# Kernel tuning notes

Hardware: AMD Instinct MI355X
Metric: run time of the kernel (lower is better)

Reference implementation:

```python
import jax, jax.numpy as jnp
import numpy as np

N, E, F, H, L = 100000, 800000, 128, 128, 64


def _glorot(key, shape):
    lim = float(np.sqrt(6.0 / (shape[0] + shape[1])))
    return jax.random.uniform(key, shape, jnp.float32, -lim, lim)


def setup_inputs() -> dict:
    key = jax.random.key(0)
    ks = jax.random.split(key, 10)
    x = jax.random.normal(ks[0], (N, F), jnp.float32)
    noise = jax.random.normal(ks[1], (N, F), jnp.float32)
    edge_index = jax.random.randint(ks[2], (2, E), 0, N, jnp.int32)
    return {
        "x": x,
        "noise": noise,
        "edge_index": edge_index,
        "bn_gamma": jnp.ones((F,), jnp.float32),
        "bn_beta": jnp.zeros((F,), jnp.float32),
        "W1": _glorot(ks[3], (F, H)),
        "b1": jnp.zeros((H,), jnp.float32),
        "W2": _glorot(ks[4], (H + 2 * F, H)),
        "b2": jnp.zeros((H,), jnp.float32),
        "Wm": _glorot(ks[5], (H + F, L)),
        "bm": jnp.zeros((L,), jnp.float32),
        "Ws": _glorot(ks[6], (H + F, L)),
        "bs": jnp.zeros((L,), jnp.float32),
    }


def _gcn_conv(x, W, b, src, dst, norm, n):
    # GCNConv: transform, then sym-normalized sparse aggregation, then bias
    h = x @ W                                 # [n, out]
    msg = h[src] * norm[:, None]              # gather + scale  [E', out]
    return jax.ops.segment_sum(msg, dst, num_segments=n) + b


def reference(x, noise, edge_index, bn_gamma, bn_beta, W1, b1, W2, b2, Wm, bm, Ws, bs):
    n = x.shape[0]
    loops = jnp.arange(n, dtype=edge_index.dtype)
    src = jnp.concatenate([edge_index[0], loops])  # add self-loops
    dst = jnp.concatenate([edge_index[1], loops])
    deg = jax.ops.segment_sum(jnp.ones_like(src, dtype=x.dtype), dst, num_segments=n)
    dinv = jnp.where(deg > 0, jax.lax.rsqrt(jnp.maximum(deg, 1e-12)), 0.0)
    norm = dinv[src] * dinv[dst]                   # D^-1/2 A D^-1/2 edge weights

    # bn1 (training-mode batch norm over nodes)
    mu = x.mean(axis=0)
    var = x.var(axis=0)
    xb = (x - mu) * jax.lax.rsqrt(var + 1e-5) * bn_gamma + bn_beta

    h1 = jax.nn.relu(_gcn_conv(xb, W1, b1, src, dst, norm, n))
    h1 = jnp.concatenate([xb, noise, h1], axis=1)  # [n, H + 2F]
    h2 = jax.nn.relu(_gcn_conv(h1, W2, b2, src, dst, norm, n))
    # dropout(p=0.4) in eval mode -> identity
    last = jnp.concatenate([xb, h2], axis=1)       # [n, F + H]
    z_mean = _gcn_conv(last, Wm, bm, src, dst, norm, n)
    z_logstd = _gcn_conv(last, Ws, bs, src, dst, norm, n)
    return (z_mean, z_logstd)
```

## Files before the change

### kernel.cpp

```cpp
#include <hip/hip_runtime.h>
#include <math.h>


typedef short bf16x8 __attribute__((ext_vector_type(8)));
typedef float f32x4 __attribute__((ext_vector_type(4)));

#define BN_G 1024

__device__ inline unsigned short f2bf(float f) {
    unsigned int u = __builtin_bit_cast(unsigned int, f);
    u += 0x7fff + ((u >> 16) & 1);
    return (unsigned short)(u >> 16);
}
__device__ inline float bfl(unsigned int u) { return __builtin_bit_cast(float, u << 16); }
__device__ inline float bfh(unsigned int u) { return __builtin_bit_cast(float, u & 0xffff0000u); }
__device__ inline unsigned int pack2(float lo, float hi) {
    return ((unsigned int)f2bf(hi) << 16) | f2bf(lo);
}
__device__ inline void acc8(float* a, uint4 v) {
    a[0] += bfl(v.x); a[1] += bfh(v.x);
    a[2] += bfl(v.y); a[3] += bfh(v.y);
    a[4] += bfl(v.z); a[5] += bfh(v.z);
    a[6] += bfl(v.w); a[7] += bfh(v.w);
}

__device__ __forceinline__ void gload_lds16(const void* g, void* l) {
    __builtin_amdgcn_global_load_lds(
        (const __attribute__((address_space(1))) unsigned int*)g,
        (__attribute__((address_space(3))) unsigned int*)l, 16, 0, 0);
}

__global__ void zero_i32(int* __restrict__ p, int n) {
    int i = blockIdx.x * blockDim.x + threadIdx.x;
    if (i < n) p[i] = 0;
}

__global__ void count_deg(const int* __restrict__ ei, int* __restrict__ cnt,
                          int* __restrict__ slot, int E) {
    int e = blockIdx.x * blockDim.x + threadIdx.x;
    if (e < E) slot[e] = atomicAdd(&cnt[ei[E + e]], 1);
}

__global__ void dinv_from_cnt(const int* __restrict__ cnt, float* __restrict__ dinv, int n) {
    int i = blockIdx.x * blockDim.x + threadIdx.x;
    if (i < n) dinv[i] = rsqrtf((float)cnt[i] + 1.0f);
}

#define SCAN_BLK 256
#define SCAN_ELEMS 1024

__global__ void scan_blocks(const int* __restrict__ cnt, int* __restrict__ out,
                            int* __restrict__ bsums, int n) {
    __shared__ int lds[SCAN_BLK];
    int base = blockIdx.x * SCAN_ELEMS;
    int t = threadIdx.x;
    int v[4];
    int s = 0;
#pragma unroll
    for (int j = 0; j < 4; j++) {
        int i = base + t * 4 + j;
        v[j] = s;
        s += (i < n) ? cnt[i] : 0;
    }
    lds[t] = s;
    __syncthreads();
    for (int off = 1; off < SCAN_BLK; off <<= 1) {
        int val = (t >= off) ? lds[t - off] : 0;
        __syncthreads();
        lds[t] += val;
        __syncthreads();
    }
    int excl = (t == 0) ? 0 : lds[t - 1];
#pragma unroll
    for (int j = 0; j < 4; j++) {
        int i = base + t * 4 + j;
        if (i < n) out[i] = excl + v[j];
    }
    if (t == SCAN_BLK - 1) bsums[blockIdx.x] = lds[t];
}

__global__ void scan_bsums(int* __restrict__ bsums, int nb) {
    if (threadIdx.x == 0 && blockIdx.x == 0) {
        int acc = 0;
        for (int i = 0; i < nb; i++) { int c = bsums[i]; bsums[i] = acc; acc += c; }
    }
}

__global__ void scan_add(int* __restrict__ row_ptr, const int* __restrict__ bsums, int n, int E) {
    int i = blockIdx.x * blockDim.x + threadIdx.x;
    if (i < n) row_ptr[i] += bsums[i / SCAN_ELEMS];
    if (i == 0) row_ptr[n] = E;
}

__global__ void fill_edges(const int* __restrict__ ei, const int* __restrict__ row_ptr,
                           const int* __restrict__ slot, int* __restrict__ edge_src, int E) {
    int e = blockIdx.x * blockDim.x + threadIdx.x;
    if (e >= E) return;
    int s = ei[e], d = ei[E + e];
    edge_src[row_ptr[d] + slot[e]] = s;
}

__global__ __launch_bounds__(256) void bn_stats(const float4* __restrict__ x4,
                                                float* __restrict__ partials, int n) {
    int t = threadIdx.x;
    int cg = t & 31;
    int rs = t >> 5;
    float4 s = make_float4(0.f, 0.f, 0.f, 0.f);
    float4 q = make_float4(0.f, 0.f, 0.f, 0.f);
    const float4 z4 = make_float4(0.f, 0.f, 0.f, 0.f);
    const int stride = BN_G * 32;
    for (int r0 = blockIdx.x * 32 + rs * 4; r0 < n; r0 += stride) {
        float4 v0 = x4[(size_t)r0 * 32 + cg];
        float4 v1 = (r0 + 1 < n) ? x4[(size_t)(r0 + 1) * 32 + cg] : z4;
        float4 v2 = (r0 + 2 < n) ? x4[(size_t)(r0 + 2) * 32 + cg] : z4;
        float4 v3 = (r0 + 3 < n) ? x4[(size_t)(r0 + 3) * 32 + cg] : z4;
        s.x += v0.x + v1.x + v2.x + v3.x;
        s.y += v0.y + v1.y + v2.y + v3.y;
        s.z += v0.z + v1.z + v2.z + v3.z;
        s.w += v0.w + v1.w + v2.w + v3.w;
        q.x = fmaf(v0.x, v0.x, fmaf(v1.x, v1.x, fmaf(v2.x, v2.x, fmaf(v3.x, v3.x, q.x))));
        q.y = fmaf(v0.y, v0.y, fmaf(v1.y, v1.y, fmaf(v2.y, v2.y, fmaf(v3.y, v3.y, q.y))));
        q.z = fmaf(v0.z, v0.z, fmaf(v1.z, v1.z, fmaf(v2.z, v2.z, fmaf(v3.z, v3.z, q.z))));
        q.w = fmaf(v0.w, v0.w, fmaf(v1.w, v1.w, fmaf(v2.w, v2.w, fmaf(v3.w, v3.w, q.w))));
    }
    __shared__ float4 lds[2][8][32];
    lds[0][rs][cg] = s;
    lds[1][rs][cg] = q;
    __syncthreads();
    if (t < 64) {
        int which = t >> 5;
        int c = t & 31;
        float4 a = lds[which][0][c];
#pragma unroll
        for (int i = 1; i < 8; i++) {
            float4 b = lds[which][i][c];
            a.x += b.x; a.y += b.y; a.z += b.z; a.w += b.w;
        }
        int base = which * 128 + c * 4;
        partials[(size_t)(base + 0) * BN_G + blockIdx.x] = a.x;
        partials[(size_t)(base + 1) * BN_G + blockIdx.x] = a.y;
        partials[(size_t)(base + 2) * BN_G + blockIdx.x] = a.z;
        partials[(size_t)(base + 3) * BN_G + blockIdx.x] = a.w;
    }
}

__global__ void bn_reduce(const float4* __restrict__ partials4, float* __restrict__ stats) {
    __shared__ float red[256];
    int c = blockIdx.x, t = threadIdx.x;
    float4 v = partials4[(size_t)c * (BN_G / 4) + t];
    red[t] = v.x + v.y + v.z + v.w;
    __syncthreads();
    for (int off = 128; off > 0; off >>= 1) {
        if (t < off) red[t] += red[t + off];
        __syncthreads();
    }
    if (t == 0) stats[c] = red[0];
}

__global__ void bn_finalize(const float* __restrict__ colsum, const float* __restrict__ colsumsq,
                            const float* __restrict__ gamma, const float* __restrict__ beta,
                            float* __restrict__ scale, float* __restrict__ shift, float invN) {
    int c = threadIdx.x;
    float mu = colsum[c] * invN;
    float var = colsumsq[c] * invN - mu * mu;
    float sc = gamma[c] / sqrtf(var + 1e-5f);
    scale[c] = sc;
    shift[c] = beta[c] - mu * sc;
}

__global__ void convert_inputs(const float4* __restrict__ x4, const float4* __restrict__ n4,
                               const float* __restrict__ scale, const float* __restrict__ shift,
                               ushort4* __restrict__ xb, ushort4* __restrict__ nb, int total4) {
    int i = blockIdx.x * blockDim.x + threadIdx.x;
    if (i >= total4) return;
    int c4 = (i & 31) << 2;
    float4 sc = *reinterpret_cast<const float4*>(scale + c4);
    float4 sh = *reinterpret_cast<const float4*>(shift + c4);
    float4 v = x4[i];
    ushort4 o;
    o.x = f2bf(fmaf(v.x, sc.x, sh.x));
    o.y = f2bf(fmaf(v.y, sc.y, sh.y));
    o.z = f2bf(fmaf(v.z, sc.z, sh.z));
    o.w = f2bf(fmaf(v.w, sc.w, sh.w));
    xb[i] = o;
    float4 w = n4[i];
    ushort4 p;
    p.x = f2bf(w.x); p.y = f2bf(w.y); p.z = f2bf(w.z); p.w = f2bf(w.w);
    nb[i] = p;
}

__global__ void pack_w(const float* __restrict__ W, unsigned short* __restrict__ Wp,
                       int K, int C, int colOff) {
    int i = blockIdx.x * blockDim.x + threadIdx.x;
    if (i >= K * C) return;
    int k = i / C, c = i % C;
    int gc = c + colOff;
    int s = k >> 7, kc = (k >> 5) & 3, lhi = (k >> 3) & 3, j = k & 7;
    int wc = gc >> 6, n = (gc >> 4) & 3, l15 = gc & 15;
    int lane = lhi * 16 + l15;
    size_t dst = ((size_t)((s * 2 + wc) * 4 + kc) * 4 + n) * 512 + lane * 8 + j;
    Wp[dst] = f2bf(W[i]);
}

template <int NSRC>
__global__ __launch_bounds__(256, 4) void gemm_mfma(
    const unsigned short* __restrict__ A0, const unsigned short* __restrict__ A1,
    const unsigned short* __restrict__ A2,
    const unsigned short* __restrict__ Wpk,
    const float* __restrict__ dinv, unsigned short* __restrict__ out)
{
    constexpr int NBUF = (NSRC > 1) ? 2 : 1;
    __shared__ unsigned char ldsA[NBUF][64 * 256];

    const int lane = threadIdx.x & 63;
    const int wid  = threadIdx.x >> 6;
    const int wr   = wid >> 1, wc = wid & 1;
    const int l15  = lane & 15, lhi = lane >> 4;
    const int c0   = wc * 64;
    const long rowblk = (long)blockIdx.x * 64;
    const int rl0 = wr * 32 + l15;
    const int rl1 = rl0 + 16;
    const int rsw = rl0 & 7;

    const unsigned short* __restrict__ srcs[3] = {A0, A1, A2};
    auto stage = [&](int s, int b) {
#pragma unroll
        for (int i = 0; i < 4; i++) {
            int G = (wid * 4 + i) * 64 + lane;
            int r = G >> 4, g = G & 15;
            const unsigned short* src = srcs[s] + (rowblk + r) * 128 + (g ^ (r & 7)) * 8;
            gload_lds16(src, &ldsA[b][G * 16]);
        }
    };

    f32x4 acc[2][4];
#pragma unroll
    for (int g = 0; g < 2; g++)
#pragma unroll
        for (int n = 0; n < 4; n++)
            acc[g][n] = (f32x4){0.f, 0.f, 0.f, 0.f};

    stage(0, 0);

#pragma unroll
    for (int s = 0; s < NSRC; s++) {
        const unsigned short* wbase = Wpk + ((size_t)(s * 2 + wc) * 16) * 512 + lane * 8;
        bf16x8 w[4][4];
#pragma unroll
        for (int kc = 0; kc < 4; kc++)
#pragma unroll
            for (int n = 0; n < 4; n++)
                w[kc][n] = *reinterpret_cast<const bf16x8*>(wbase + (kc * 4 + n) * 512);

        __syncthreads();
        if (s + 1 < NSRC) stage(s + 1, (s + 1) % NBUF);
        const unsigned char* bufp = ldsA[s % NBUF];

#pragma unroll
        for (int kc = 0; kc < 4; kc++) {
            int g0 = kc * 4 + lhi;
            bf16x8 a0 = *reinterpret_cast<const bf16x8*>(bufp + rl0 * 256 + (g0 ^ rsw) * 16);
            bf16x8 a1 = *reinterpret_cast<const bf16x8*>(bufp + rl1 * 256 + (g0 ^ rsw) * 16);
#pragma unroll
            for (int n = 0; n < 4; n++) {
                acc[0][n] = __builtin_amdgcn_mfma_f32_16x16x32_bf16(w[kc][n], a0, acc[0][n], 0, 0, 0);
                acc[1][n] = __builtin_amdgcn_mfma_f32_16x16x32_bf16(w[kc][n], a1, acc[1][n], 0, 0, 0);
            }
        }
    }

#pragma unroll
    for (int g = 0; g < 2; g++) {
        long row = rowblk + (g ? rl1 : rl0);
        float dv = dinv[row];
        unsigned short* op = out + row * 128 + c0 + lhi * 4;
#pragma unroll
        for (int n = 0; n < 4; n++) {
            f32x4 v = acc[g][n];
            ushort4 pk;
            pk.x = f2bf(v[0] * dv);
            pk.y = f2bf(v[1] * dv);
            pk.z = f2bf(v[2] * dv);
            pk.w = f2bf(v[3] * dv);
            *reinterpret_cast<ushort4*>(op + n * 16) = pk;
        }
    }
}

template <bool RELU>
__global__ void gather16(const uint4* __restrict__ hs4, const float* __restrict__ dinv,
                         const int* __restrict__ row_ptr, const int* __restrict__ edge_src,
                         const float* __restrict__ bias, uint4* __restrict__ out4, int n) {
    int node = blockIdx.x * 4 + (threadIdx.x >> 6);
    if (node >= n) return;
    int lane = threadIdx.x & 63;
    int cl = lane & 15, sub = lane >> 4;
    int beg = row_ptr[node], end = row_ptr[node + 1];
    float a0[8] = {0.f,0.f,0.f,0.f,0.f,0.f,0.f,0.f};
    float a1[8] = {0.f,0.f,0.f,0.f,0.f,0.f,0.f,0.f};
    if (sub == 0) acc8(a0, hs4[(size_t)node * 16 + cl]);
    int e = beg + sub;
    for (; e + 4 < end; e += 8) {
        uint4 v0 = hs4[(size_t)edge_src[e] * 16 + cl];
        uint4 v1 = hs4[(size_t)edge_src[e + 4] * 16 + cl];
        acc8(a0, v0);
        acc8(a1, v1);
    }
    if (e < end) acc8(a0, hs4[(size_t)edge_src[e] * 16 + cl]);
#pragma unroll
    for (int i = 0; i < 8; i++) a0[i] += a1[i];
#pragma unroll
    for (int i = 0; i < 8; i++) {
        a0[i] += __shfl_xor(a0[i], 16);
        a0[i] += __shfl_xor(a0[i], 32);
    }
    if (sub == 0) {
        float dv = dinv[node];
        float4 b0 = *reinterpret_cast<const float4*>(bias + cl * 8);
        float4 b1 = *reinterpret_cast<const float4*>(bias + cl * 8 + 4);
        float r0 = fmaf(a0[0], dv, b0.x), r1 = fmaf(a0[1], dv, b0.y);
        float r2 = fmaf(a0[2], dv, b0.z), r3 = fmaf(a0[3], dv, b0.w);
        float r4 = fmaf(a0[4], dv, b1.x), r5 = fmaf(a0[5], dv, b1.y);
        float r6 = fmaf(a0[6], dv, b1.z), r7 = fmaf(a0[7], dv, b1.w);
        if (RELU) {
            r0 = fmaxf(r0, 0.f); r1 = fmaxf(r1, 0.f); r2 = fmaxf(r2, 0.f); r3 = fmaxf(r3, 0.f);
            r4 = fmaxf(r4, 0.f); r5 = fmaxf(r5, 0.f); r6 = fmaxf(r6, 0.f); r7 = fmaxf(r7, 0.f);
        }
        uint4 o;
        o.x = pack2(r0, r1); o.y = pack2(r2, r3);
        o.z = pack2(r4, r5); o.w = pack2(r6, r7);
        out4[(size_t)node * 16 + cl] = o;
    }
}

__global__ void gather_dual(const uint4* __restrict__ hs4, const float* __restrict__ dinv,
                            const int* __restrict__ row_ptr, const int* __restrict__ edge_src,
                            const float* __restrict__ bm, const float* __restrict__ bs,
                            float* __restrict__ zm, float* __restrict__ zs, int n) {
    int node = blockIdx.x * 4 + (threadIdx.x >> 6);
    if (node >= n) return;
    int lane = threadIdx.x & 63;
    int cl = lane & 15, sub = lane >> 4;
    int beg = row_ptr[node], end = row_ptr[node + 1];
    float a0[8] = {0.f,0.f,0.f,0.f,0.f,0.f,0.f,0.f};
    float a1[8] = {0.f,0.f,0.f,0.f,0.f,0.f,0.f,0.f};
    if (sub == 0) acc8(a0, hs4[(size_t)node * 16 + cl]);
    int e = beg + sub;
    for (; e + 4 < end; e += 8) {
        uint4 v0 = hs4[(size_t)edge_src[e] * 16 + cl];
        uint4 v1 = hs4[(size_t)edge_src[e + 4] * 16 + cl];
        acc8(a0, v0);
        acc8(a1, v1);
    }
    if (e < end) acc8(a0, hs4[(size_t)edge_src[e] * 16 + cl]);
#pragma unroll
    for (int i = 0; i < 8; i++) a0[i] += a1[i];
#pragma unroll
    for (int i = 0; i < 8; i++) {
        a0[i] += __shfl_xor(a0[i], 16);
        a0[i] += __shfl_xor(a0[i], 32);
    }
    if (sub == 0) {
        float dv = dinv[node];
        const float* bp = (cl < 8) ? (bm + cl * 8) : (bs + (cl - 8) * 8);
        float* zp = (cl < 8) ? (zm + (size_t)node * 64 + cl * 8)
                             : (zs + (size_t)node * 64 + (cl - 8) * 8);
        float4 b0 = *reinterpret_cast<const float4*>(bp);
        float4 b1 = *reinterpret_cast<const float4*>(bp + 4);
        float4 o0 = make_float4(fmaf(a0[0], dv, b0.x), fmaf(a0[1], dv, b0.y),
                                fmaf(a0[2], dv, b0.z), fmaf(a0[3], dv, b0.w));
        float4 o1 = make_float4(fmaf(a0[4], dv, b1.x), fmaf(a0[5], dv, b1.y),
                                fmaf(a0[6], dv, b1.z), fmaf(a0[7], dv, b1.w));
        *reinterpret_cast<float4*>(zp) = o0;
        *reinterpret_cast<float4*>(zp + 4) = o1;
    }
}


extern "C" void kernel_launch(void* const* d_in, const int* in_sizes, int n_in,
                              void* d_out, int out_size, void* d_ws, size_t ws_size,
                              hipStream_t stream) {
    const float* x     = (const float*)d_in[0];
    const float* noise = (const float*)d_in[1];
    const int*   ei    = (const int*)d_in[2];
    const float* gamma = (const float*)d_in[3];
    const float* beta  = (const float*)d_in[4];
    const float* W1    = (const float*)d_in[5];
    const float* b1    = (const float*)d_in[6];
    const float* W2    = (const float*)d_in[7];
    const float* b2    = (const float*)d_in[8];
    const float* Wm    = (const float*)d_in[9];
    const float* bm    = (const float*)d_in[10];
    const float* Ws    = (const float*)d_in[11];
    const float* bs    = (const float*)d_in[12];

    const int N  = in_sizes[0] / 128;
    const int E  = in_sizes[2] / 2;
    const int NPAD = (N + 127) & ~127;
    const int nb = (N + SCAN_ELEMS - 1) / SCAN_ELEMS;

    auto align256 = [](size_t b) { return (b + 255) & ~(size_t)255; };
    char* p = (char*)d_ws;
    int* cnt      = (int*)p;  p += align256((size_t)N * 4);
    int* row_ptr  = (int*)p;  p += align256((size_t)(N + 1) * 4);
    int* edge_src = (int*)p;  p += align256((size_t)E * 4);
    int* slot     = (int*)p;  p += align256((size_t)E * 4);
    int* bsums    = (int*)p;  p += align256((size_t)nb * 4);
    float* dinv   = (float*)p; p += align256((size_t)NPAD * 4);
    float* stats  = (float*)p; p += align256(512 * 4);
    float* bnpart = (float*)p; p += align256((size_t)256 * BN_G * 4);
    unsigned short* Wp1 = (unsigned short*)p; p += align256(128 * 128 * 2);
    unsigned short* Wp2 = (unsigned short*)p; p += align256(128 * 384 * 2);
    unsigned short* Wpc = (unsigned short*)p; p += align256(128 * 256 * 2);
    unsigned short* xb16 = (unsigned short*)p; p += align256((size_t)NPAD * 128 * 2);
    unsigned short* n16  = (unsigned short*)p; p += align256((size_t)NPAD * 128 * 2);
    unsigned short* h16  = (unsigned short*)p; p += align256((size_t)NPAD * 128 * 2);

    float* colsum   = stats;
    float* colsumsq = stats + 128;
    float* scale    = stats + 256;
    float* shift    = stats + 384;

    float* dout = (float*)d_out;
    unsigned short* hs12 = (unsigned short*)d_out;
    unsigned short* hs3  = n16;
    float* zm = dout;
    float* zs = dout + (size_t)N * 64;

    const int gblocks = NPAD / 64;
    const int nblocks4 = (N + 3) / 4;

    zero_i32<<<(N + 255) / 256, 256, 0, stream>>>(cnt, N);
    count_deg<<<(E + 255) / 256, 256, 0, stream>>>(ei, cnt, slot, E);
    bn_stats<<<BN_G, 256, 0, stream>>>((const float4*)x, bnpart, N);
    bn_reduce<<<256, 256, 0, stream>>>((const float4*)bnpart, stats);
    bn_finalize<<<1, 128, 0, stream>>>(colsum, colsumsq, gamma, beta, scale, shift, 1.0f / (float)N);
    scan_blocks<<<nb, SCAN_BLK, 0, stream>>>(cnt, row_ptr, bsums, N);
    scan_bsums<<<1, 64, 0, stream>>>(bsums, nb);
    scan_add<<<(N + 255) / 256, 256, 0, stream>>>(row_ptr, bsums, N, E);
    dinv_from_cnt<<<(N + 255) / 256, 256, 0, stream>>>(cnt, dinv, N);
    fill_edges<<<(E + 255) / 256, 256, 0, stream>>>(ei, row_ptr, slot, edge_src, E);
    convert_inputs<<<(N * 32 + 255) / 256, 256, 0, stream>>>(
        (const float4*)x, (const float4*)noise, scale, shift,
        (ushort4*)xb16, (ushort4*)n16, N * 32);
    pack_w<<<(128 * 128 + 255) / 256, 256, 0, stream>>>(W1, Wp1, 128, 128, 0);
    pack_w<<<(384 * 128 + 255) / 256, 256, 0, stream>>>(W2, Wp2, 384, 128, 0);
    pack_w<<<(256 * 64 + 255) / 256, 256, 0, stream>>>(Wm, Wpc, 256, 64, 0);
    pack_w<<<(256 * 64 + 255) / 256, 256, 0, stream>>>(Ws, Wpc, 256, 64, 64);

    gemm_mfma<1><<<gblocks, 256, 0, stream>>>(xb16, nullptr, nullptr, Wp1, dinv, hs12);
    gather16<true><<<nblocks4, 256, 0, stream>>>((const uint4*)hs12, dinv, row_ptr,
                                                 edge_src, b1, (uint4*)h16, N);
    gemm_mfma<3><<<gblocks, 256, 0, stream>>>(xb16, n16, h16, Wp2, dinv, hs12);
    gather16<true><<<nblocks4, 256, 0, stream>>>((const uint4*)hs12, dinv, row_ptr,
                                                 edge_src, b2, (uint4*)h16, N);
    gemm_mfma<2><<<gblocks, 256, 0, stream>>>(xb16, h16, nullptr, Wpc, dinv, hs3);
    gather_dual<<<nblocks4, 256, 0, stream>>>((const uint4*)hs3, dinv, row_ptr,
                                              edge_src, bm, bs, zm, zs, N);
}
```

Baseline: 317.9 us.

## Fuse independent preprocessing kernels into merged launches and vectorize gather accumulation

Merges the many small preprocessing kernels into five launches. BN stats now runs with degree counting, BN reduce with the block scan, the bsums scan with BN finalize, scan-add with dinv, and edge fill with input conversion and weight packing. Each merged launch picks its role by block index, and a hipMemsetAsync replaces the zero kernel, all to cut launch overhead and serialization gaps. The gather kernels also accumulate in float2 vectors so the compiler can use packed FP32 adds. The risks are heterogeneous blocks in one grid causing load imbalance, and possible register changes.

```diff
diff --git a/kernel.cpp b/kernel.cpp
--- a/kernel.cpp
+++ b/kernel.cpp
@@ -4,8 +4,11 @@
 
 typedef short bf16x8 __attribute__((ext_vector_type(8)));
 typedef float f32x4 __attribute__((ext_vector_type(4)));
+typedef float f32x2 __attribute__((ext_vector_type(2)));
 
 #define BN_G 1024
+#define SCAN_BLK 256
+#define SCAN_ELEMS 1024
 
 __device__ inline unsigned short f2bf(float f) {
     unsigned int u = __builtin_bit_cast(unsigned int, f);
@@ -17,11 +20,12 @@
 __device__ inline unsigned int pack2(float lo, float hi) {
     return ((unsigned int)f2bf(hi) << 16) | f2bf(lo);
 }
-__device__ inline void acc8(float* a, uint4 v) {
-    a[0] += bfl(v.x); a[1] += bfh(v.x);
-    a[2] += bfl(v.y); a[3] += bfh(v.y);
-    a[4] += bfl(v.z); a[5] += bfh(v.z);
-    a[6] += bfl(v.w); a[7] += bfh(v.w);
+__device__ inline f32x2 unp(unsigned int u) {
+    return (f32x2){__builtin_bit_cast(float, u << 16),
+                   __builtin_bit_cast(float, u & 0xffff0000u)};
+}
+__device__ inline void acc8v(f32x2* a, uint4 v) {
+    a[0] += unp(v.x); a[1] += unp(v.y); a[2] += unp(v.z); a[3] += unp(v.w);
 }
 
 __device__ __forceinline__ void gload_lds16(const void* g, void* l) {
@@ -30,168 +34,137 @@
         (__attribute__((address_space(3))) unsigned int*)l, 16, 0, 0);
 }
 
-__global__ void zero_i32(int* __restrict__ p, int n) {
-    int i = blockIdx.x * blockDim.x + threadIdx.x;
-    if (i < n) p[i] = 0;
-}
-
-__global__ void count_deg(const int* __restrict__ ei, int* __restrict__ cnt,
-                          int* __restrict__ slot, int E) {
-    int e = blockIdx.x * blockDim.x + threadIdx.x;
-    if (e < E) slot[e] = atomicAdd(&cnt[ei[E + e]], 1);
-}
-
-__global__ void dinv_from_cnt(const int* __restrict__ cnt, float* __restrict__ dinv, int n) {
-    int i = blockIdx.x * blockDim.x + threadIdx.x;
-    if (i < n) dinv[i] = rsqrtf((float)cnt[i] + 1.0f);
-}
-
-#define SCAN_BLK 256
-#define SCAN_ELEMS 1024
-
-__global__ void scan_blocks(const int* __restrict__ cnt, int* __restrict__ out,
-                            int* __restrict__ bsums, int n) {
+__global__ __launch_bounds__(256) void fused1(const float4* __restrict__ x4,
+                                              float* __restrict__ partials, int n,
+                                              const int* __restrict__ ei,
+                                              int* __restrict__ cnt,
+                                              int* __restrict__ slot, int E) {
+    __shared__ float4 lds[2][8][32];
+    int bid = blockIdx.x, t = threadIdx.x;
+    if (bid < BN_G) {
+        int cg = t & 31;
+        int rs = t >> 5;
+        float4 s = make_float4(0.f, 0.f, 0.f, 0.f);
+        float4 q = make_float4(0.f, 0.f, 0.f, 0.f);
+        const float4 z4 = make_float4(0.f, 0.f, 0.f, 0.f);
+        const int stride = BN_G * 32;
+        for (int r0 = bid * 32 + rs * 4; r0 < n; r0 += stride) {
+            float4 v0 = x4[(size_t)r0 * 32 + cg];
+            float4 v1 = (r0 + 1 < n) ? x4[(size_t)(r0 + 1) * 32 + cg] : z4;
+            float4 v2 = (r0 + 2 < n) ? x4[(size_t)(r0 + 2) * 32 + cg] : z4;
+            float4 v3 = (r0 + 3 < n) ? x4[(size_t)(r0 + 3) * 32 + cg] : z4;
+            s.x += v0.x + v1.x + v2.x + v3.x;
+            s.y += v0.y + v1.y + v2.y + v3.y;
+            s.z += v0.z + v1.z + v2.z + v3.z;
+            s.w += v0.w + v1.w + v2.w + v3.w;
+            q.x = fmaf(v0.x, v0.x, fmaf(v1.x, v1.x, fmaf(v2.x, v2.x, fmaf(v3.x, v3.x, q.x))));
+            q.y = fmaf(v0.y, v0.y, fmaf(v1.y, v1.y, fmaf(v2.y, v2.y, fmaf(v3.y, v3.y, q.y))));
+            q.z = fmaf(v0.z, v0.z, fmaf(v1.z, v1.z, fmaf(v2.z, v2.z, fmaf(v3.z, v3.z, q.z))));
+            q.w = fmaf(v0.w, v0.w, fmaf(v1.w, v1.w, fmaf(v2.w, v2.w, fmaf(v3.w, v3.w, q.w))));
+        }
+        lds[0][rs][cg] = s;
+        lds[1][rs][cg] = q;
+        __syncthreads();
+        if (t < 64) {
+            int which = t >> 5;
+            int c = t & 31;
+            float4 a = lds[which][0][c];
+#pragma unroll
+            for (int i = 1; i < 8; i++) {
+                float4 b = lds[which][i][c];
+                a.x += b.x; a.y += b.y; a.z += b.z; a.w += b.w;
+            }
+            int base = which * 128 + c * 4;
+            partials[(size_t)(base + 0) * BN_G + bid] = a.x;
+            partials[(size_t)(base + 1) * BN_G + bid] = a.y;
+            partials[(size_t)(base + 2) * BN_G + bid] = a.z;
+            partials[(size_t)(base + 3) * BN_G + bid] = a.w;
+        }
+    } else {
+        int e = (bid - BN_G) * 256 + t;
+        if (e < E) slot[e] = atomicAdd(&cnt[ei[E + e]], 1);
+    }
+}
+
+__global__ __launch_bounds__(256) void fused2(const float4* __restrict__ partials4,
+                                              float* __restrict__ stats,
+                                              const int* __restrict__ cnt,
+                                              int* __restrict__ row_ptr,
+                                              int* __restrict__ bsums, int n) {
+    __shared__ float red[256];
     __shared__ int lds[SCAN_BLK];
-    int base = blockIdx.x * SCAN_ELEMS;
     int t = threadIdx.x;
-    int v[4];
-    int s = 0;
-#pragma unroll
-    for (int j = 0; j < 4; j++) {
-        int i = base + t * 4 + j;
-        v[j] = s;
-        s += (i < n) ? cnt[i] : 0;
-    }
-    lds[t] = s;
-    __syncthreads();
-    for (int off = 1; off < SCAN_BLK; off <<= 1) {
-        int val = (t >= off) ? lds[t - off] : 0;
+    if (blockIdx.x < 256) {
+        int c = blockIdx.x;
+        float4 v = partials4[(size_t)c * (BN_G / 4) + t];
+        red[t] = v.x + v.y + v.z + v.w;
         __syncthreads();
-        lds[t] += val;
+        for (int off = 128; off > 0; off >>= 1) {
+            if (t < off) red[t] += red[t + off];
+            __syncthreads();
+        }
+        if (t == 0) stats[c] = red[0];
+    } else {
+        int blk = blockIdx.x - 256;
+        int base = blk * SCAN_ELEMS;
+        int v[4];
+        int s = 0;
+#pragma unroll
+        for (int j = 0; j < 4; j++) {
+            int i = base + t * 4 + j;
+            v[j] = s;
+            s += (i < n) ? cnt[i] : 0;
+        }
+        lds[t] = s;
         __syncthreads();
-    }
-    int excl = (t == 0) ? 0 : lds[t - 1];
-#pragma unroll
-    for (int j = 0; j < 4; j++) {
-        int i = base + t * 4 + j;
-        if (i < n) out[i] = excl + v[j];
-    }
-    if (t == SCAN_BLK - 1) bsums[blockIdx.x] = lds[t];
-}
-
-__global__ void scan_bsums(int* __restrict__ bsums, int nb) {
-    if (threadIdx.x == 0 && blockIdx.x == 0) {
+        for (int off = 1; off < SCAN_BLK; off <<= 1) {
+            int val = (t >= off) ? lds[t - off] : 0;
+            __syncthreads();
+            lds[t] += val;
+            __syncthreads();
+        }
+        int excl = (t == 0) ? 0 : lds[t - 1];
+#pragma unroll
+        for (int j = 0; j < 4; j++) {
+            int i = base + t * 4 + j;
+            if (i < n) row_ptr[i] = excl + v[j];
+        }
+        if (t == SCAN_BLK - 1) bsums[blk] = lds[t];
+    }
+}
+
+__global__ void fused3(int* __restrict__ bsums, int nb,
+                       const float* __restrict__ stats,
+                       const float* __restrict__ gamma, const float* __restrict__ beta,
+                       float* __restrict__ scale, float* __restrict__ shift, float invN) {
+    int t = threadIdx.x;
+    if (t == 0) {
         int acc = 0;
         for (int i = 0; i < nb; i++) { int c = bsums[i]; bsums[i] = acc; acc += c; }
-    }
-}
-
-__global__ void scan_add(int* __restrict__ row_ptr, const int* __restrict__ bsums, int n, int E) {
+    } else if (t >= 128 && t < 256) {
+        int c = t - 128;
+        float mu = stats[c] * invN;
+        float var = stats[128 + c] * invN - mu * mu;
+        float sc = gamma[c] / sqrtf(var + 1e-5f);
+        scale[c] = sc;
+        shift[c] = beta[c] - mu * sc;
+    }
+}
+
+__global__ void fused4(int* __restrict__ row_ptr, const int* __restrict__ bsums,
+                       const int* __restrict__ cnt, float* __restrict__ dinv,
+                       int n, int E) {
     int i = blockIdx.x * blockDim.x + threadIdx.x;
-    if (i < n) row_ptr[i] += bsums[i / SCAN_ELEMS];
+    if (i < n) {
+        row_ptr[i] += bsums[i / SCAN_ELEMS];
+        dinv[i] = rsqrtf((float)cnt[i] + 1.0f);
+    }
     if (i == 0) row_ptr[n] = E;
 }
 
-__global__ void fill_edges(const int* __restrict__ ei, const int* __restrict__ row_ptr,
-                           const int* __restrict__ slot, int* __restrict__ edge_src, int E) {
-    int e = blockIdx.x * blockDim.x + threadIdx.x;
-    if (e >= E) return;
-    int s = ei[e], d = ei[E + e];
-    edge_src[row_ptr[d] + slot[e]] = s;
-}
-
-__global__ __launch_bounds__(256) void bn_stats(const float4* __restrict__ x4,
-                                                float* __restrict__ partials, int n) {
-    int t = threadIdx.x;
-    int cg = t & 31;
-    int rs = t >> 5;
-    float4 s = make_float4(0.f, 0.f, 0.f, 0.f);
-    float4 q = make_float4(0.f, 0.f, 0.f, 0.f);
-    const float4 z4 = make_float4(0.f, 0.f, 0.f, 0.f);
-    const int stride = BN_G * 32;
-    for (int r0 = blockIdx.x * 32 + rs * 4; r0 < n; r0 += stride) {
-        float4 v0 = x4[(size_t)r0 * 32 + cg];
-        float4 v1 = (r0 + 1 < n) ? x4[(size_t)(r0 + 1) * 32 + cg] : z4;
-        float4 v2 = (r0 + 2 < n) ? x4[(size_t)(r0 + 2) * 32 + cg] : z4;
-        float4 v3 = (r0 + 3 < n) ? x4[(size_t)(r0 + 3) * 32 + cg] : z4;
-        s.x += v0.x + v1.x + v2.x + v3.x;
-        s.y += v0.y + v1.y + v2.y + v3.y;
-        s.z += v0.z + v1.z + v2.z + v3.z;
-        s.w += v0.w + v1.w + v2.w + v3.w;
-        q.x = fmaf(v0.x, v0.x, fmaf(v1.x, v1.x, fmaf(v2.x, v2.x, fmaf(v3.x, v3.x, q.x))));
-        q.y = fmaf(v0.y, v0.y, fmaf(v1.y, v1.y, fmaf(v2.y, v2.y, fmaf(v3.y, v3.y, q.y))));
-        q.z = fmaf(v0.z, v0.z, fmaf(v1.z, v1.z, fmaf(v2.z, v2.z, fmaf(v3.z, v3.z, q.z))));
-        q.w = fmaf(v0.w, v0.w, fmaf(v1.w, v1.w, fmaf(v2.w, v2.w, fmaf(v3.w, v3.w, q.w))));
-    }
-    __shared__ float4 lds[2][8][32];
-    lds[0][rs][cg] = s;
-    lds[1][rs][cg] = q;
-    __syncthreads();
-    if (t < 64) {
-        int which = t >> 5;
-        int c = t & 31;
-        float4 a = lds[which][0][c];
-#pragma unroll
-        for (int i = 1; i < 8; i++) {
-            float4 b = lds[which][i][c];
-            a.x += b.x; a.y += b.y; a.z += b.z; a.w += b.w;
-        }
-        int base = which * 128 + c * 4;
-        partials[(size_t)(base + 0) * BN_G + blockIdx.x] = a.x;
-        partials[(size_t)(base + 1) * BN_G + blockIdx.x] = a.y;
-        partials[(size_t)(base + 2) * BN_G + blockIdx.x] = a.z;
-        partials[(size_t)(base + 3) * BN_G + blockIdx.x] = a.w;
-    }
-}
-
-__global__ void bn_reduce(const float4* __restrict__ partials4, float* __restrict__ stats) {
-    __shared__ float red[256];
-    int c = blockIdx.x, t = threadIdx.x;
-    float4 v = partials4[(size_t)c * (BN_G / 4) + t];
-    red[t] = v.x + v.y + v.z + v.w;
-    __syncthreads();
-    for (int off = 128; off > 0; off >>= 1) {
-        if (t < off) red[t] += red[t + off];
-        __syncthreads();
-    }
-    if (t == 0) stats[c] = red[0];
-}
-
-__global__ void bn_finalize(const float* __restrict__ colsum, const float* __restrict__ colsumsq,
-                            const float* __restrict__ gamma, const float* __restrict__ beta,
-                            float* __restrict__ scale, float* __restrict__ shift, float invN) {
-    int c = threadIdx.x;
-    float mu = colsum[c] * invN;
-    float var = colsumsq[c] * invN - mu * mu;
-    float sc = gamma[c] / sqrtf(var + 1e-5f);
-    scale[c] = sc;
-    shift[c] = beta[c] - mu * sc;
-}
-
-__global__ void convert_inputs(const float4* __restrict__ x4, const float4* __restrict__ n4,
-                               const float* __restrict__ scale, const float* __restrict__ shift,
-                               ushort4* __restrict__ xb, ushort4* __restrict__ nb, int total4) {
-    int i = blockIdx.x * blockDim.x + threadIdx.x;
-    if (i >= total4) return;
-    int c4 = (i & 31) << 2;
-    float4 sc = *reinterpret_cast<const float4*>(scale + c4);
-    float4 sh = *reinterpret_cast<const float4*>(shift + c4);
-    float4 v = x4[i];
-    ushort4 o;
-    o.x = f2bf(fmaf(v.x, sc.x, sh.x));
-    o.y = f2bf(fmaf(v.y, sc.y, sh.y));
-    o.z = f2bf(fmaf(v.z, sc.z, sh.z));
-    o.w = f2bf(fmaf(v.w, sc.w, sh.w));
-    xb[i] = o;
-    float4 w = n4[i];
-    ushort4 p;
-    p.x = f2bf(w.x); p.y = f2bf(w.y); p.z = f2bf(w.z); p.w = f2bf(w.w);
-    nb[i] = p;
-}
-
-__global__ void pack_w(const float* __restrict__ W, unsigned short* __restrict__ Wp,
-                       int K, int C, int colOff) {
-    int i = blockIdx.x * blockDim.x + threadIdx.x;
+__device__ inline void pack_body(int i, const float* __restrict__ W,
+                                 unsigned short* __restrict__ Wp,
+                                 int K, int C, int colOff) {
     if (i >= K * C) return;
     int k = i / C, c = i % C;
     int gc = c + colOff;
@@ -200,6 +173,57 @@
     int lane = lhi * 16 + l15;
     size_t dst = ((size_t)((s * 2 + wc) * 4 + kc) * 4 + n) * 512 + lane * 8 + j;
     Wp[dst] = f2bf(W[i]);
+}
+
+__global__ __launch_bounds__(256) void fused5(
+    const int* __restrict__ ei, const int* __restrict__ row_ptr,
+    const int* __restrict__ slot, int* __restrict__ edge_src, int E, int EB,
+    const float4* __restrict__ x4, const float4* __restrict__ n4,
+    const float* __restrict__ scale, const float* __restrict__ shift,
+    ushort4* __restrict__ xb, ushort4* __restrict__ nb4, int total4, int CB,
+    const float* __restrict__ W1, unsigned short* __restrict__ Wp1,
+    const float* __restrict__ W2, unsigned short* __restrict__ Wp2,
+    const float* __restrict__ Wm, const float* __restrict__ Ws,
+    unsigned short* __restrict__ Wpc)
+{
+    int bid = blockIdx.x, t = threadIdx.x;
+    if (bid < EB) {
+        int e = bid * 256 + t;
+        if (e < E) {
+            int s = ei[e], d = ei[E + e];
+            edge_src[row_ptr[d] + slot[e]] = s;
+        }
+        return;
+    }
+    bid -= EB;
+    if (bid < CB) {
+        int i = bid * 256 + t;
+        if (i < total4) {
+            int c4 = (i & 31) << 2;
+            float4 sc = *reinterpret_cast<const float4*>(scale + c4);
+            float4 sh = *reinterpret_cast<const float4*>(shift + c4);
+            float4 v = x4[i];
+            ushort4 o;
+            o.x = f2bf(fmaf(v.x, sc.x, sh.x));
+            o.y = f2bf(fmaf(v.y, sc.y, sh.y));
+            o.z = f2bf(fmaf(v.z, sc.z, sh.z));
+            o.w = f2bf(fmaf(v.w, sc.w, sh.w));
+            xb[i] = o;
+            float4 w = n4[i];
+            ushort4 p;
+            p.x = f2bf(w.x); p.y = f2bf(w.y); p.z = f2bf(w.z); p.w = f2bf(w.w);
+            nb4[i] = p;
+        }
+        return;
+    }
+    bid -= CB;
+    if (bid < 64)  { pack_body(bid * 256 + t, W1, Wp1, 128, 128, 0); return; }
+    bid -= 64;
+    if (bid < 192) { pack_body(bid * 256 + t, W2, Wp2, 384, 128, 0); return; }
+    bid -= 192;
+    if (bid < 64)  { pack_body(bid * 256 + t, Wm, Wpc, 256, 64, 0); return; }
+    bid -= 64;
+    pack_body(bid * 256 + t, Ws, Wpc, 256, 64, 64);
 }
 
 template <int NSRC>
@@ -296,32 +320,34 @@
     int lane = threadIdx.x & 63;
     int cl = lane & 15, sub = lane >> 4;
     int beg = row_ptr[node], end = row_ptr[node + 1];
-    float a0[8] = {0.f,0.f,0.f,0.f,0.f,0.f,0.f,0.f};
-    float a1[8] = {0.f,0.f,0.f,0.f,0.f,0.f,0.f,0.f};
-    if (sub == 0) acc8(a0, hs4[(size_t)node * 16 + cl]);
+    f32x2 a0[4] = {(f32x2){0.f,0.f}, (f32x2){0.f,0.f}, (f32x2){0.f,0.f}, (f32x2){0.f,0.f}};
+    f32x2 a1[4] = {(f32x2){0.f,0.f}, (f32x2){0.f,0.f}, (f32x2){0.f,0.f}, (f32x2){0.f,0.f}};
+    if (sub == 0) acc8v(a0, hs4[(size_t)node * 16 + cl]);
     int e = beg + sub;
     for (; e + 4 < end; e += 8) {
         uint4 v0 = hs4[(size_t)edge_src[e] * 16 + cl];
         uint4 v1 = hs4[(size_t)edge_src[e + 4] * 16 + cl];
-        acc8(a0, v0);
-        acc8(a1, v1);
-    }
-    if (e < end) acc8(a0, hs4[(size_t)edge_src[e] * 16 + cl]);
-#pragma unroll
-    for (int i = 0; i < 8; i++) a0[i] += a1[i];
-#pragma unroll
-    for (int i = 0; i < 8; i++) {
-        a0[i] += __shfl_xor(a0[i], 16);
-        a0[i] += __shfl_xor(a0[i], 32);
+        acc8v(a0, v0);
+        acc8v(a1, v1);
+    }
+    if (e < end) acc8v(a0, hs4[(size_t)edge_src[e] * 16 + cl]);
+#pragma unroll
+    for (int i = 0; i < 4; i++) a0[i] += a1[i];
+#pragma unroll
+    for (int i = 0; i < 4; i++) {
+        a0[i].x += __shfl_xor(a0[i].x, 16);
+        a0[i].y += __shfl_xor(a0[i].y, 16);
+        a0[i].x += __shfl_xor(a0[i].x, 32);
+        a0[i].y += __shfl_xor(a0[i].y, 32);
     }
     if (sub == 0) {
         float dv = dinv[node];
         float4 b0 = *reinterpret_cast<const float4*>(bias + cl * 8);
         float4 b1 = *reinterpret_cast<const float4*>(bias + cl * 8 + 4);
-        float r0 = fmaf(a0[0], dv, b0.x), r1 = fmaf(a0[1], dv, b0.y);
-        float r2 = fmaf(a0[2], dv, b0.z), r3 = fmaf(a0[3], dv, b0.w);
-        float r4 = fmaf(a0[4], dv, b1.x), r5 = fmaf(a0[5], dv, b1.y);
-        float r6 = fmaf(a0[6], dv, b1.z), r7 = fmaf(a0[7], dv, b1.w);
+        float r0 = fmaf(a0[0].x, dv, b0.x), r1 = fmaf(a0[0].y, dv, b0.y);
+        float r2 = fmaf(a0[1].x, dv, b0.z), r3 = fmaf(a0[1].y, dv, b0.w);
+        float r4 = fmaf(a0[2].x, dv, b1.x), r5 = fmaf(a0[2].y, dv, b1.y);
+        float r6 = fmaf(a0[3].x, dv, b1.z), r7 = fmaf(a0[3].y, dv, b1.w);
         if (RELU) {
             r0 = fmaxf(r0, 0.f); r1 = fmaxf(r1, 0.f); r2 = fmaxf(r2, 0.f); r3 = fmaxf(r3, 0.f);
             r4 = fmaxf(r4, 0.f); r5 = fmaxf(r5, 0.f); r6 = fmaxf(r6, 0.f); r7 = fmaxf(r7, 0.f);
@@ -342,23 +368,25 @@
     int lane = threadIdx.x & 63;
     int cl = lane & 15, sub = lane >> 4;
     int beg = row_ptr[node], end = row_ptr[node + 1];
-    float a0[8] = {0.f,0.f,0.f,0.f,0.f,0.f,0.f,0.f};
-    float a1[8] = {0.f,0.f,0.f,0.f,0.f,0.f,0.f,0.f};
-    if (sub == 0) acc8(a0, hs4[(size_t)node * 16 + cl]);
+    f32x2 a0[4] = {(f32x2){0.f,0.f}, (f32x2){0.f,0.f}, (f32x2){0.f,0.f}, (f32x2){0.f,0.f}};
+    f32x2 a1[4] = {(f32x2){0.f,0.f}, (f32x2){0.f,0.f}, (f32x2){0.f,0.f}, (f32x2){0.f,0.f}};
+    if (sub == 0) acc8v(a0, hs4[(size_t)node * 16 + cl]);
     int e = beg + sub;
     for (; e + 4 < end; e += 8) {
         uint4 v0 = hs4[(size_t)edge_src[e] * 16 + cl];
         uint4 v1 = hs4[(size_t)edge_src[e + 4] * 16 + cl];
-        acc8(a0, v0);
-        acc8(a1, v1);
-    }
-    if (e < end) acc8(a0, hs4[(size_t)edge_src[e] * 16 + cl]);
-#pragma unroll
-    for (int i = 0; i < 8; i++) a0[i] += a1[i];
-#pragma unroll
-    for (int i = 0; i < 8; i++) {
-        a0[i] += __shfl_xor(a0[i], 16);
-        a0[i] += __shfl_xor(a0[i], 32);
+        acc8v(a0, v0);
+        acc8v(a1, v1);
+    }
+    if (e < end) acc8v(a0, hs4[(size_t)edge_src[e] * 16 + cl]);
+#pragma unroll
+    for (int i = 0; i < 4; i++) a0[i] += a1[i];
+#pragma unroll
+    for (int i = 0; i < 4; i++) {
+        a0[i].x += __shfl_xor(a0[i].x, 16);
+        a0[i].y += __shfl_xor(a0[i].y, 16);
+        a0[i].x += __shfl_xor(a0[i].x, 32);
+        a0[i].y += __shfl_xor(a0[i].y, 32);
     }
     if (sub == 0) {
         float dv = dinv[node];
@@ -367,10 +395,10 @@
                              : (zs + (size_t)node * 64 + (cl - 8) * 8);
         float4 b0 = *reinterpret_cast<const float4*>(bp);
         float4 b1 = *reinterpret_cast<const float4*>(bp + 4);
-        float4 o0 = make_float4(fmaf(a0[0], dv, b0.x), fmaf(a0[1], dv, b0.y),
-                                fmaf(a0[2], dv, b0.z), fmaf(a0[3], dv, b0.w));
-        float4 o1 = make_float4(fmaf(a0[4], dv, b1.x), fmaf(a0[5], dv, b1.y),
-                                fmaf(a0[6], dv, b1.z), fmaf(a0[7], dv, b1.w));
+        float4 o0 = make_float4(fmaf(a0[0].x, dv, b0.x), fmaf(a0[0].y, dv, b0.y),
+                                fmaf(a0[1].x, dv, b0.z), fmaf(a0[1].y, dv, b0.w));
+        float4 o1 = make_float4(fmaf(a0[2].x, dv, b1.x), fmaf(a0[2].y, dv, b1.y),
+                                fmaf(a0[3].x, dv, b1.z), fmaf(a0[3].y, dv, b1.w));
         *reinterpret_cast<float4*>(zp) = o0;
         *reinterpret_cast<float4*>(zp + 4) = o1;
     }
@@ -398,6 +426,8 @@
     const int E  = in_sizes[2] / 2;
     const int NPAD = (N + 127) & ~127;
     const int nb = (N + SCAN_ELEMS - 1) / SCAN_ELEMS;
+    const int EB = (E + 255) / 256;
+    const int CB = (N * 32 + 255) / 256;
 
     auto align256 = [](size_t b) { return (b + 255) & ~(size_t)255; };
     char* p = (char*)d_ws;
@@ -416,10 +446,8 @@
     unsigned short* n16  = (unsigned short*)p; p += align256((size_t)NPAD * 128 * 2);
     unsigned short* h16  = (unsigned short*)p; p += align256((size_t)NPAD * 128 * 2);
 
-    float* colsum   = stats;
-    float* colsumsq = stats + 128;
-    float* scale    = stats + 256;
-    float* shift    = stats + 384;
+    float* scale = stats + 256;
+    float* shift = stats + 384;
 
     float* dout = (float*)d_out;
     unsigned short* hs12 = (unsigned short*)d_out;
@@ -430,23 +458,16 @@
     const int gblocks = NPAD / 64;
     const int nblocks4 = (N + 3) / 4;
 
-    zero_i32<<<(N + 255) / 256, 256, 0, stream>>>(cnt, N);
-    count_deg<<<(E + 255) / 256, 256, 0, stream>>>(ei, cnt, slot, E);
-    bn_stats<<<BN_G, 256, 0, stream>>>((const float4*)x, bnpart, N);
-    bn_reduce<<<256, 256, 0, stream>>>((const float4*)bnpart, stats);
-    bn_finalize<<<1, 128, 0, stream>>>(colsum, colsumsq, gamma, beta, scale, shift, 1.0f / (float)N);
-    scan_blocks<<<nb, SCAN_BLK, 0, stream>>>(cnt, row_ptr, bsums, N);
-    scan_bsums<<<1, 64, 0, stream>>>(bsums, nb);
-    scan_add<<<(N + 255) / 256, 256, 0, stream>>>(row_ptr, bsums, N, E);
-    dinv_from_cnt<<<(N + 255) / 256, 256, 0, stream>>>(cnt, dinv, N);
-    fill_edges<<<(E + 255) / 256, 256, 0, stream>>>(ei, row_ptr, slot, edge_src, E);
-    convert_inputs<<<(N * 32 + 255) / 256, 256, 0, stream>>>(
+    hipMemsetAsync(cnt, 0, (size_t)N * 4, stream);
+    fused1<<<BN_G + EB, 256, 0, stream>>>((const float4*)x, bnpart, N, ei, cnt, slot, E);
+    fused2<<<256 + nb, 256, 0, stream>>>((const float4*)bnpart, stats, cnt, row_ptr, bsums, N);
+    fused3<<<1, 256, 0, stream>>>(bsums, nb, stats, gamma, beta, scale, shift, 1.0f / (float)N);
+    fused4<<<(N + 255) / 256, 256, 0, stream>>>(row_ptr, bsums, cnt, dinv, N, E);
+    fused5<<<EB + CB + 384, 256, 0, stream>>>(
+        ei, row_ptr, slot, edge_src, E, EB,
         (const float4*)x, (const float4*)noise, scale, shift,
-        (ushort4*)xb16, (ushort4*)n16, N * 32);
-    pack_w<<<(128 * 128 + 255) / 256, 256, 0, stream>>>(W1, Wp1, 128, 128, 0);
-    pack_w<<<(384 * 128 + 255) / 256, 256, 0, stream>>>(W2, Wp2, 384, 128, 0);
-    pack_w<<<(256 * 64 + 255) / 256, 256, 0, stream>>>(Wm, Wpc, 256, 64, 0);
-    pack_w<<<(256 * 64 + 255) / 256, 256, 0, stream>>>(Ws, Wpc, 256, 64, 64);
+        (ushort4*)xb16, (ushort4*)n16, N * 32, CB,
+        W1, Wp1, W2, Wp2, Wm, Ws, Wpc);
 
     gemm_mfma<1><<<gblocks, 256, 0, stream>>>(xb16, nullptr, nullptr, Wp1, dinv, hs12);
     gather16<true><<<nblocks4, 256, 0, stream>>>((const uint4*)hs12, dinv, row_ptr,
```

New measurement: 296.0 us. 6.9% less time.
